# Optimization experiments

Measured on AMD Instinct MI355X. Metric: run time of the kernel, lower is better.

Reference implementation:

```python
import jax, jax.numpy as jnp
import numpy as np

B, S, L = 2, 2048, 2048
H, KVH, D = 16, 4, 128
HID = H * D
EPS = 1e-6
SCALE = 1.0 / np.sqrt(D)


def rmsnorm(x, w, eps=EPS):
    # normalize over last dim (head_size), fp32 math
    xf = x.astype(jnp.float32)
    var = jnp.mean(xf * xf, axis=-1, keepdims=True)
    return (xf * jax.lax.rsqrt(var + eps)).astype(x.dtype) * w


def setup_inputs() -> dict:
    key = jax.random.key(0)
    ks = jax.random.split(key, 5)
    s = 1.0 / np.sqrt(HID)
    return {
        "x": jax.random.normal(ks[0], (B, S, HID), jnp.float32),
        "c": jax.random.normal(ks[1], (B, L, HID), jnp.float32),
        "wq": jax.random.normal(ks[2], (HID, H * D), jnp.float32) * s,
        "wkv": jax.random.normal(ks[3], (HID, KVH * D * 2), jnp.float32) * s,
        "wo": jax.random.normal(ks[4], (H * D, HID), jnp.float32) * s,
        "norm_q_w": jnp.ones((D,), jnp.float32),
        "norm_k_w": jnp.ones((D,), jnp.float32),
    }


def reference(x, c, wq, wkv, wo, norm_q_w, norm_k_w):
    bs, seq_len, _ = x.shape
    c_len = c.shape[1]
    n_rep = H // KVH
    # Q projection + per-head RMSNorm
    xq = (x @ wq).reshape(bs, seq_len, H, D)
    xq = rmsnorm(xq, norm_q_w)
    # packed KV projection: view(..., kvh, hd, 2), unbind last dim
    ckv = (c @ wkv).reshape(bs, c_len, KVH, D, 2)
    ck, cv = ckv[..., 0], ckv[..., 1]
    ck = rmsnorm(ck, norm_k_w)
    # GQA repeat_kv (repeat_interleave over head dim)
    ck = jnp.repeat(ck, n_rep, axis=2)  # [b, L, H, D]
    cv = jnp.repeat(cv, n_rep, axis=2)
    # SDPA cross-attention, softmax in fp32
    scores = jnp.einsum("bqhd,bkhd->bhqk", xq, ck) * SCALE
    attn = jax.nn.softmax(scores.astype(jnp.float32), axis=-1).astype(xq.dtype)
    out = jnp.einsum("bhqk,bkhd->bqhd", attn, cv)
    out = out.reshape(bs, seq_len, H * D)
    return out @ wo
```

## Files before the change

### kernel.cpp

```cpp
#include <hip/hip_runtime.h>

#define B_ 2
#define S_ 2048
#define L_ 2048
#define H_ 16
#define KVH_ 4
#define D_ 128
#define HID_ 2048
#define EPS_ 1e-6f

typedef unsigned short u16;
typedef unsigned int u32;
typedef __bf16 bf16x8 __attribute__((ext_vector_type(8)));
typedef float f32x4 __attribute__((ext_vector_type(4)));
typedef unsigned u32x2v __attribute__((ext_vector_type(2)));
typedef unsigned u32x4v __attribute__((ext_vector_type(4)));

__device__ __forceinline__ float bf2f(u32 u) {
  union { u32 i; float f; } x; x.i = u << 16; return x.f;
}
__device__ __forceinline__ u16 f2bf(float f) {
  union { float f; u32 i; } x; x.f = f;
  return (u16)((x.i + 0x7fffu + ((x.i >> 16) & 1u)) >> 16);
}
__device__ __forceinline__ u32 pack_bf16(float a, float b) {
#if __has_builtin(__builtin_amdgcn_cvt_pk_bf16_f32)
  typedef __bf16 bf16x2 __attribute__((ext_vector_type(2)));
  union { bf16x2 v; u32 u; } c;
  c.v = __builtin_amdgcn_cvt_pk_bf16_f32(a, b);
  return c.u;
#else
  return (u32)f2bf(a) | ((u32)f2bf(b) << 16);
#endif
}
__device__ __forceinline__ void gl2lds16(const u16* g, u16* l) {
  __builtin_amdgcn_global_load_lds(
      (const __attribute__((address_space(1))) u32*)g,
      (__attribute__((address_space(3))) u32*)l, 16, 0, 0);
}

#if __has_builtin(__builtin_amdgcn_permlane32_swap) && __has_builtin(__builtin_amdgcn_permlane16_swap)
#define HAS_PLS 1
#else
#define HAS_PLS 0
#endif

__device__ __forceinline__ u32x4v ctoa(u32 xa, u32 xb, u32 ya, u32 yb,
                                       int quad, int l15) {
  u32x4v f;
#if HAS_PLS
  u32x2v t1 = __builtin_amdgcn_permlane32_swap(xa, ya, false, false);
  u32x2v t2 = __builtin_amdgcn_permlane16_swap(t1.x, t1.y, false, false);
  u32x2v t3 = __builtin_amdgcn_permlane32_swap(xb, yb, false, false);
  u32x2v t4 = __builtin_amdgcn_permlane16_swap(t3.x, t3.y, false, false);
  f.x = t2.x; f.y = t4.x; f.z = t2.y; f.w = t4.y;
#else
  int a0 = (((2 * quad) & 3) * 16 + l15) << 2;
  int a1 = (((2 * quad + 1) & 3) * 16 + l15) << 2;
  u32 xa0 = __builtin_amdgcn_ds_bpermute(a0, xa), ya0 = __builtin_amdgcn_ds_bpermute(a0, ya);
  u32 xb0 = __builtin_amdgcn_ds_bpermute(a0, xb), yb0 = __builtin_amdgcn_ds_bpermute(a0, yb);
  u32 xa1 = __builtin_amdgcn_ds_bpermute(a1, xa), ya1 = __builtin_amdgcn_ds_bpermute(a1, ya);
  u32 xb1 = __builtin_amdgcn_ds_bpermute(a1, xb), yb1 = __builtin_amdgcn_ds_bpermute(a1, yb);
  bool hi = quad >= 2;
  f.x = hi ? ya0 : xa0; f.y = hi ? yb0 : xb0;
  f.z = hi ? ya1 : xa1; f.w = hi ? yb1 : xb1;
#endif
  return f;
}

__global__ __launch_bounds__(256) void cvt_bf16(const float* __restrict__ in,
                                                u16* __restrict__ out, int n4) {
  int i = blockIdx.x * 256 + threadIdx.x;
  if (i >= n4) return;
  float4 v = ((const float4*)in)[i];
  uint2 o;
  o.x = pack_bf16(v.x, v.y);
  o.y = pack_bf16(v.z, v.w);
  ((uint2*)out)[i] = o;
}

__global__ __launch_bounds__(256) void transp_bf16(const float* __restrict__ A,
                                                   u16* __restrict__ At, int R, int C) {
  __shared__ float t[64][65];
  int c0 = blockIdx.x * 64, r0 = blockIdx.y * 64;
  int tx = threadIdx.x & 63, ty = threadIdx.x >> 6;
  for (int i = ty; i < 64; i += 4)
    t[i][tx] = A[(size_t)(r0 + i) * C + c0 + tx];
  __syncthreads();
  for (int i = ty; i < 64; i += 4)
    At[(size_t)(c0 + i) * R + r0 + tx] = f2bf(t[tx][i]);
}

__device__ __forceinline__ void store_out(u16* p, float v) { *p = f2bf(v); }
__device__ __forceinline__ void store_out(float* p, float v) { *p = v; }

template <typename OutT>
__global__ __launch_bounds__(256, 2) void gemm_bt(const u16* __restrict__ A,
                                                  const u16* __restrict__ Bt,
                                                  OutT* __restrict__ C,
                                                  int M, int N, int K) {
  __shared__ u16 sA[128 * 32];
  __shared__ u16 sB[128 * 32];
  const int tid = threadIdx.x;
  const int wave = tid >> 6, lane = tid & 63;
  const int quad = lane >> 4, l15 = lane & 15;
  const int m0 = blockIdx.x * 128, n0 = blockIdx.y * 128;
  const int wm = (wave >> 1) * 64, wn = (wave & 1) * 64;
  const u16* aP = A + (size_t)m0 * K;
  const u16* bP = Bt + (size_t)n0 * K;
  const int sr = lane >> 2;
  const int sc = (lane & 3) * 8;
  const int r0 = wave * 32, r1 = wave * 32 + 16;

  f32x4 acc[4][4];
  for (int i = 0; i < 4; i++)
    for (int j = 0; j < 4; j++)
      for (int r = 0; r < 4; r++) acc[i][j][r] = 0.0f;

  for (int k0 = 0; k0 < K; k0 += 32) {
    gl2lds16(aP + (size_t)(r0 + sr) * K + k0 + sc, &sA[r0 * 32]);
    gl2lds16(aP + (size_t)(r1 + sr) * K + k0 + sc, &sA[r1 * 32]);
    gl2lds16(bP + (size_t)(r0 + sr) * K + k0 + sc, &sB[r0 * 32]);
    gl2lds16(bP + (size_t)(r1 + sr) * K + k0 + sc, &sB[r1 * 32]);
    __syncthreads();
    bf16x8 afrag[4], bfrag[4];
    for (int i = 0; i < 4; i++)
      afrag[i] = *(const bf16x8*)&sA[(wm + i * 16 + l15) * 32 + quad * 8];
    for (int j = 0; j < 4; j++)
      bfrag[j] = *(const bf16x8*)&sB[(wn + j * 16 + l15) * 32 + quad * 8];
    for (int i = 0; i < 4; i++)
      for (int j = 0; j < 4; j++)
        acc[i][j] = __builtin_amdgcn_mfma_f32_16x16x32_bf16(afrag[i], bfrag[j], acc[i][j], 0, 0, 0);
    __syncthreads();
  }
  for (int i = 0; i < 4; i++)
    for (int j = 0; j < 4; j++) {
      int row = m0 + wm + i * 16 + quad * 4;
      int col = n0 + wn + j * 16 + l15;
      for (int r = 0; r < 4; r++)
        store_out(&C[(size_t)(row + r) * N + col], acc[i][j][r]);
    }
}

__global__ __launch_bounds__(256) void rmsnorm_q(u16* __restrict__ XQ,
                                                 const float* __restrict__ w) {
  int gw = blockIdx.x * 4 + (threadIdx.x >> 6);
  int lane = threadIdx.x & 63;
  u16* base = XQ + (size_t)gw * 128;
  float x0 = bf2f(base[lane]), x1 = bf2f(base[lane + 64]);
  float ss = x0 * x0 + x1 * x1;
  for (int off = 1; off < 64; off <<= 1) ss += __shfl_xor(ss, off);
  const float cexp = 0.12753102331322172f;
  float scale = rsqrtf(ss * (1.0f / 128.0f) + EPS_) * cexp;
  base[lane] = f2bf(x0 * scale * w[lane]);
  base[lane + 64] = f2bf(x1 * scale * w[lane + 64]);
}

__global__ __launch_bounds__(256) void knorm_deint(const u16* __restrict__ CKV,
                                                   const float* __restrict__ w,
                                                   u16* __restrict__ K,
                                                   u16* __restrict__ Vt) {
  __shared__ u16 vbuf[128][66];
  const int tid = threadIdx.x, wave = tid >> 6, lane = tid & 63;
  const int l0 = blockIdx.x * 64, kvh = blockIdx.y, b = blockIdx.z;
  for (int it = 0; it < 16; it++) {
    int ll = wave * 16 + it;
    int row = b * L_ + l0 + ll;
    const u16* src = CKV + (size_t)row * 1024 + kvh * 256;
    u32 p0 = *(const u32*)&src[lane * 2];
    u32 p1 = *(const u32*)&src[(lane + 64) * 2];
    float k0 = bf2f(p0 & 0xffff), v0 = bf2f(p0 >> 16);
    float k1 = bf2f(p1 & 0xffff), v1 = bf2f(p1 >> 16);
    float ss = k0 * k0 + k1 * k1;
    for (int off = 1; off < 64; off <<= 1) ss += __shfl_xor(ss, off);
    float sc = rsqrtf(ss * (1.0f / 128.0f) + EPS_);
    size_t kb = (((size_t)b * KVH_ + kvh) * L_ + l0 + ll) * D_;
    K[kb + lane] = f2bf(k0 * sc * w[lane]);
    K[kb + lane + 64] = f2bf(k1 * sc * w[lane + 64]);
    vbuf[lane][ll] = f2bf(v0);
    vbuf[lane + 64][ll] = f2bf(v1);
  }
  __syncthreads();
  for (int it = tid; it < 128 * 32; it += 256) {
    int d = it >> 5, cc = (it & 31) * 2;
    u32 pk = (u32)vbuf[d][cc] | ((u32)vbuf[d][cc + 1] << 16);
    *(u32*)&Vt[(((size_t)b * KVH_ + kvh) * D_ + d) * L_ + l0 + cc] = pk;
  }
}

__global__ __launch_bounds__(256, 4) void attn(const u16* __restrict__ Q,
                                               const u16* __restrict__ K,
                                               const u16* __restrict__ Vt,
                                               u16* __restrict__ AO) {
  __shared__ u16 sk[4][64 * 32];
  __shared__ u16 sv[2][128 * 32];
  const int tid = threadIdx.x, wave = tid >> 6, lane = tid & 63;
  const int quad = lane >> 4, l15 = lane & 15;
  const int qt = blockIdx.x, h = blockIdx.y, b = blockIdx.z;
  const int kvh = h >> 2;
  const int s0 = qt * 64, wr0 = wave * 16;

  const u16* qrow = Q + (size_t)(b * S_ + s0 + wr0 + l15) * HID_ + h * D_;
  bf16x8 qf[4];
  for (int kc = 0; kc < 4; kc++)
    qf[kc] = *(const bf16x8*)&qrow[kc * 32 + quad * 8];

  float psum = 0.0f;
  f32x4 o[8];
  for (int n = 0; n < 8; n++)
    for (int r = 0; r < 4; r++) o[n][r] = 0.0f;

  const u16* kbase = K + ((size_t)(b * KVH_ + kvh) * L_) * D_;
  const u16* vbase = Vt + ((size_t)(b * KVH_ + kvh) * D_) * L_;
  const int srow = lane >> 2, scol = (lane & 3) * 8;

  for (int l0 = 0; l0 < L_; l0 += 64) {
    const u16* kb = kbase + (size_t)l0 * D_ + wave * 32;
    for (int is = 0; is < 4; is++)
      gl2lds16(kb + (size_t)(is * 16 + srow) * D_ + scol, &sk[wave][is * 16 * 32]);
    const int c = wave >> 1;
    const u16* vb = vbase + l0 + c * 32;
    for (int j = 0; j < 4; j++) {
      int dr = (wave & 1) * 64 + j * 16;
      gl2lds16(vb + (size_t)(dr + srow) * L_ + scol, &sv[c][dr * 32]);
    }
    __syncthreads();

    f32x4 sacc[4];
    for (int j = 0; j < 4; j++)
      for (int r = 0; r < 4; r++) sacc[j][r] = 0.0f;
    for (int j = 0; j < 4; j++)
      for (int kc = 0; kc < 4; kc++) {
        bf16x8 kf = *(const bf16x8*)&sk[kc][(j * 16 + l15) * 32 + quad * 8];
        sacc[j] = __builtin_amdgcn_mfma_f32_16x16x32_bf16(kf, qf[kc], sacc[j], 0, 0, 0);
      }

    u32 pa[4], pb[4];
    for (int j = 0; j < 4; j++) {
      float p0 = exp2f(sacc[j][0]), p1 = exp2f(sacc[j][1]);
      float p2 = exp2f(sacc[j][2]), p3 = exp2f(sacc[j][3]);
      psum += (p0 + p1) + (p2 + p3);
      pa[j] = pack_bf16(p0, p1);
      pb[j] = pack_bf16(p2, p3);
    }

    for (int cc = 0; cc < 2; cc++) {
      union { u32x4v u; bf16x8 v; } pf;
      pf.u = ctoa(pa[2 * cc], pb[2 * cc], pa[2 * cc + 1], pb[2 * cc + 1], quad, l15);
      for (int n = 0; n < 8; n++) {
        bf16x8 vf = *(const bf16x8*)&sv[cc][(n * 16 + l15) * 32 + quad * 8];
        o[n] = __builtin_amdgcn_mfma_f32_16x16x32_bf16(pf.v, vf, o[n], 0, 0, 0);
      }
    }
    __syncthreads();
  }

  psum += __shfl_xor(psum, 16);
  psum += __shfl_xor(psum, 32);
  float linv = 1.0f / psum;
  float lr[4];
  for (int r = 0; r < 4; r++) lr[r] = __shfl(linv, quad * 4 + r);
  u16* ob = AO + (size_t)(b * S_ + s0 + wr0) * HID_ + h * D_;
  for (int n = 0; n < 8; n++)
    for (int r = 0; r < 4; r++)
      ob[(size_t)(quad * 4 + r) * HID_ + n * 16 + l15] = f2bf(o[n][r] * lr[r]);
}

extern "C" void kernel_launch(void* const* d_in, const int* in_sizes, int n_in,
                              void* d_out, int out_size, void* d_ws, size_t ws_size,
                              hipStream_t stream) {
  const float* x = (const float*)d_in[0];
  const float* c = (const float*)d_in[1];
  const float* wq = (const float*)d_in[2];
  const float* wkv = (const float*)d_in[3];
  const float* wo = (const float*)d_in[4];
  const float* nqw = (const float*)d_in[5];
  const float* nkw = (const float*)d_in[6];
  float* out = (float*)d_out;

  const int M = B_ * S_;
  char* p = (char*)d_ws;
  auto alloc = [&](size_t bytes) {
    char* r = p;
    p += (bytes + 255) & ~(size_t)255;
    return r;
  };
  u16* xbf = (u16*)alloc((size_t)M * HID_ * 2);
  u16* cbf = (u16*)alloc((size_t)M * HID_ * 2);
  u16* wqT = (u16*)alloc((size_t)HID_ * HID_ * 2);
  u16* wkvT = (u16*)alloc((size_t)1024 * HID_ * 2);
  u16* woT = (u16*)alloc((size_t)HID_ * HID_ * 2);
  u16* XQ = (u16*)alloc((size_t)M * HID_ * 2);
  u16* CKV = (u16*)alloc((size_t)M * 1024 * 2);
  u16* Kb = (u16*)alloc((size_t)B_ * KVH_ * L_ * D_ * 2);
  u16* Vt = (u16*)alloc((size_t)B_ * KVH_ * D_ * L_ * 2);
  u16* AO = (u16*)alloc((size_t)M * HID_ * 2);

  cvt_bf16<<<8192, 256, 0, stream>>>(x, xbf, M * HID_ / 4);
  cvt_bf16<<<8192, 256, 0, stream>>>(c, cbf, M * HID_ / 4);
  transp_bf16<<<dim3(32, 32), 256, 0, stream>>>(wq, wqT, HID_, HID_);
  transp_bf16<<<dim3(16, 32), 256, 0, stream>>>(wkv, wkvT, HID_, 1024);
  transp_bf16<<<dim3(32, 32), 256, 0, stream>>>(wo, woT, HID_, HID_);
  gemm_bt<u16><<<dim3(32, 16), 256, 0, stream>>>(xbf, wqT, XQ, M, HID_, HID_);
  gemm_bt<u16><<<dim3(32, 8), 256, 0, stream>>>(cbf, wkvT, CKV, M, 1024, HID_);
  rmsnorm_q<<<16384, 256, 0, stream>>>(XQ, nqw);
  knorm_deint<<<dim3(32, 4, 2), 256, 0, stream>>>(CKV, nkw, Kb, Vt);
  attn<<<dim3(32, 16, 2), 256, 0, stream>>>(XQ, Kb, Vt, AO);
  gemm_bt<float><<<dim3(32, 16), 256, 0, stream>>>(AO, woT, out, M, HID_, HID_);
}
```

Before: 419.7 us.

## Fuse Q RMSNorm into attention and double query/key tile per block

Result: faster. 401.2 us (-4.4%).

```diff
diff --git a/kernel.cpp b/kernel.cpp
--- a/kernel.cpp
+++ b/kernel.cpp
@@ -140,20 +140,6 @@
       for (int r = 0; r < 4; r++)
         store_out(&C[(size_t)(row + r) * N + col], acc[i][j][r]);
     }
-}
-
-__global__ __launch_bounds__(256) void rmsnorm_q(u16* __restrict__ XQ,
-                                                 const float* __restrict__ w) {
-  int gw = blockIdx.x * 4 + (threadIdx.x >> 6);
-  int lane = threadIdx.x & 63;
-  u16* base = XQ + (size_t)gw * 128;
-  float x0 = bf2f(base[lane]), x1 = bf2f(base[lane + 64]);
-  float ss = x0 * x0 + x1 * x1;
-  for (int off = 1; off < 64; off <<= 1) ss += __shfl_xor(ss, off);
-  const float cexp = 0.12753102331322172f;
-  float scale = rsqrtf(ss * (1.0f / 128.0f) + EPS_) * cexp;
-  base[lane] = f2bf(x0 * scale * w[lane]);
-  base[lane + 64] = f2bf(x1 * scale * w[lane + 64]);
 }
 
 __global__ __launch_bounds__(256) void knorm_deint(const u16* __restrict__ CKV,
@@ -188,82 +174,118 @@
   }
 }
 
-__global__ __launch_bounds__(256, 4) void attn(const u16* __restrict__ Q,
+__global__ __launch_bounds__(256, 2) void attn(const u16* __restrict__ XQ,
+                                               const float* __restrict__ nw,
                                                const u16* __restrict__ K,
                                                const u16* __restrict__ Vt,
                                                u16* __restrict__ AO) {
-  __shared__ u16 sk[4][64 * 32];
-  __shared__ u16 sv[2][128 * 32];
+  __shared__ u16 sk[4][128 * 32];
+  __shared__ u16 sv[4][128 * 32];
   const int tid = threadIdx.x, wave = tid >> 6, lane = tid & 63;
   const int quad = lane >> 4, l15 = lane & 15;
   const int qt = blockIdx.x, h = blockIdx.y, b = blockIdx.z;
   const int kvh = h >> 2;
-  const int s0 = qt * 64, wr0 = wave * 16;
-
-  const u16* qrow = Q + (size_t)(b * S_ + s0 + wr0 + l15) * HID_ + h * D_;
-  bf16x8 qf[4];
-  for (int kc = 0; kc < 4; kc++)
-    qf[kc] = *(const bf16x8*)&qrow[kc * 32 + quad * 8];
-
-  float psum = 0.0f;
-  f32x4 o[8];
-  for (int n = 0; n < 8; n++)
-    for (int r = 0; r < 4; r++) o[n][r] = 0.0f;
+  const int s0 = qt * 128, wr0 = wave * 32;
+
+  bf16x8 qf[2][4];
+  {
+    const float cexp = 0.12753102331322172f;
+    const u16* qrow = XQ + (size_t)(b * S_ + s0 + wr0 + l15) * HID_ + h * D_;
+    for (int i = 0; i < 2; i++) {
+      const u16* qr = qrow + (size_t)i * 16 * HID_;
+      float vals[4][8];
+      float ss = 0.0f;
+      for (int kc = 0; kc < 4; kc++) {
+        uint4 u = *(const uint4*)&qr[kc * 32 + quad * 8];
+        u32 uu[4] = {u.x, u.y, u.z, u.w};
+        for (int e = 0; e < 4; e++) {
+          float lo = bf2f(uu[e] & 0xffff), hi = bf2f(uu[e] >> 16);
+          vals[kc][2 * e] = lo;
+          vals[kc][2 * e + 1] = hi;
+          ss += lo * lo + hi * hi;
+        }
+      }
+      ss += __shfl_xor(ss, 16);
+      ss += __shfl_xor(ss, 32);
+      float scale = rsqrtf(ss * (1.0f / 128.0f) + EPS_) * cexp;
+      for (int kc = 0; kc < 4; kc++) {
+        float4 w0 = *(const float4*)&nw[kc * 32 + quad * 8];
+        float4 w1 = *(const float4*)&nw[kc * 32 + quad * 8 + 4];
+        union { u32x4v u; bf16x8 v; } q;
+        q.u.x = pack_bf16(vals[kc][0] * scale * w0.x, vals[kc][1] * scale * w0.y);
+        q.u.y = pack_bf16(vals[kc][2] * scale * w0.z, vals[kc][3] * scale * w0.w);
+        q.u.z = pack_bf16(vals[kc][4] * scale * w1.x, vals[kc][5] * scale * w1.y);
+        q.u.w = pack_bf16(vals[kc][6] * scale * w1.z, vals[kc][7] * scale * w1.w);
+        qf[i][kc] = q.v;
+      }
+    }
+  }
+
+  float psum[2] = {0.0f, 0.0f};
+  f32x4 o[2][8];
+  for (int i = 0; i < 2; i++)
+    for (int n = 0; n < 8; n++)
+      for (int r = 0; r < 4; r++) o[i][n][r] = 0.0f;
 
   const u16* kbase = K + ((size_t)(b * KVH_ + kvh) * L_) * D_;
   const u16* vbase = Vt + ((size_t)(b * KVH_ + kvh) * D_) * L_;
   const int srow = lane >> 2, scol = (lane & 3) * 8;
 
-  for (int l0 = 0; l0 < L_; l0 += 64) {
+  for (int l0 = 0; l0 < L_; l0 += 128) {
     const u16* kb = kbase + (size_t)l0 * D_ + wave * 32;
-    for (int is = 0; is < 4; is++)
+    for (int is = 0; is < 8; is++)
       gl2lds16(kb + (size_t)(is * 16 + srow) * D_ + scol, &sk[wave][is * 16 * 32]);
-    const int c = wave >> 1;
-    const u16* vb = vbase + l0 + c * 32;
-    for (int j = 0; j < 4; j++) {
-      int dr = (wave & 1) * 64 + j * 16;
-      gl2lds16(vb + (size_t)(dr + srow) * L_ + scol, &sv[c][dr * 32]);
+    const u16* vb = vbase + l0 + wave * 32;
+    for (int is = 0; is < 8; is++)
+      gl2lds16(vb + (size_t)(is * 16 + srow) * L_ + scol, &sv[wave][is * 16 * 32]);
+    __syncthreads();
+
+    for (int cc = 0; cc < 4; cc++) {
+      f32x4 sacc[2][2];
+      for (int jj = 0; jj < 2; jj++)
+        for (int i = 0; i < 2; i++)
+          for (int r = 0; r < 4; r++) sacc[jj][i][r] = 0.0f;
+      for (int jj = 0; jj < 2; jj++) {
+        int j = cc * 2 + jj;
+        for (int kc = 0; kc < 4; kc++) {
+          bf16x8 kf = *(const bf16x8*)&sk[kc][(j * 16 + l15) * 32 + quad * 8];
+          for (int i = 0; i < 2; i++)
+            sacc[jj][i] = __builtin_amdgcn_mfma_f32_16x16x32_bf16(kf, qf[i][kc], sacc[jj][i], 0, 0, 0);
+        }
+      }
+      union { u32x4v u; bf16x8 v; } pf[2];
+      for (int i = 0; i < 2; i++) {
+        float p0[4], p1[4];
+        for (int r = 0; r < 4; r++) {
+          p0[r] = exp2f(sacc[0][i][r]);
+          p1[r] = exp2f(sacc[1][i][r]);
+          psum[i] += p0[r] + p1[r];
+        }
+        u32 xa = pack_bf16(p0[0], p0[1]), xb = pack_bf16(p0[2], p0[3]);
+        u32 ya = pack_bf16(p1[0], p1[1]), yb = pack_bf16(p1[2], p1[3]);
+        pf[i].u = ctoa(xa, xb, ya, yb, quad, l15);
+      }
+      for (int n = 0; n < 8; n++) {
+        bf16x8 vf = *(const bf16x8*)&sv[cc][(n * 16 + l15) * 32 + quad * 8];
+        for (int i = 0; i < 2; i++)
+          o[i][n] = __builtin_amdgcn_mfma_f32_16x16x32_bf16(pf[i].v, vf, o[i][n], 0, 0, 0);
+      }
     }
     __syncthreads();
-
-    f32x4 sacc[4];
-    for (int j = 0; j < 4; j++)
-      for (int r = 0; r < 4; r++) sacc[j][r] = 0.0f;
-    for (int j = 0; j < 4; j++)
-      for (int kc = 0; kc < 4; kc++) {
-        bf16x8 kf = *(const bf16x8*)&sk[kc][(j * 16 + l15) * 32 + quad * 8];
-        sacc[j] = __builtin_amdgcn_mfma_f32_16x16x32_bf16(kf, qf[kc], sacc[j], 0, 0, 0);
-      }
-
-    u32 pa[4], pb[4];
-    for (int j = 0; j < 4; j++) {
-      float p0 = exp2f(sacc[j][0]), p1 = exp2f(sacc[j][1]);
-      float p2 = exp2f(sacc[j][2]), p3 = exp2f(sacc[j][3]);
-      psum += (p0 + p1) + (p2 + p3);
-      pa[j] = pack_bf16(p0, p1);
-      pb[j] = pack_bf16(p2, p3);
-    }
-
-    for (int cc = 0; cc < 2; cc++) {
-      union { u32x4v u; bf16x8 v; } pf;
-      pf.u = ctoa(pa[2 * cc], pb[2 * cc], pa[2 * cc + 1], pb[2 * cc + 1], quad, l15);
-      for (int n = 0; n < 8; n++) {
-        bf16x8 vf = *(const bf16x8*)&sv[cc][(n * 16 + l15) * 32 + quad * 8];
-        o[n] = __builtin_amdgcn_mfma_f32_16x16x32_bf16(pf.v, vf, o[n], 0, 0, 0);
-      }
-    }
-    __syncthreads();
-  }
-
-  psum += __shfl_xor(psum, 16);
-  psum += __shfl_xor(psum, 32);
-  float linv = 1.0f / psum;
-  float lr[4];
-  for (int r = 0; r < 4; r++) lr[r] = __shfl(linv, quad * 4 + r);
-  u16* ob = AO + (size_t)(b * S_ + s0 + wr0) * HID_ + h * D_;
-  for (int n = 0; n < 8; n++)
-    for (int r = 0; r < 4; r++)
-      ob[(size_t)(quad * 4 + r) * HID_ + n * 16 + l15] = f2bf(o[n][r] * lr[r]);
+  }
+
+  for (int i = 0; i < 2; i++) {
+    float s = psum[i];
+    s += __shfl_xor(s, 16);
+    s += __shfl_xor(s, 32);
+    float linv = 1.0f / s;
+    float lr[4];
+    for (int r = 0; r < 4; r++) lr[r] = __shfl(linv, quad * 4 + r);
+    u16* ob = AO + (size_t)(b * S_ + s0 + wr0 + i * 16) * HID_ + h * D_;
+    for (int n = 0; n < 8; n++)
+      for (int r = 0; r < 4; r++)
+        ob[(size_t)(quad * 4 + r) * HID_ + n * 16 + l15] = f2bf(o[i][n][r] * lr[r]);
+  }
 }
 
 extern "C" void kernel_launch(void* const* d_in, const int* in_sizes, int n_in,
@@ -303,8 +325,7 @@
   transp_bf16<<<dim3(32, 32), 256, 0, stream>>>(wo, woT, HID_, HID_);
   gemm_bt<u16><<<dim3(32, 16), 256, 0, stream>>>(xbf, wqT, XQ, M, HID_, HID_);
   gemm_bt<u16><<<dim3(32, 8), 256, 0, stream>>>(cbf, wkvT, CKV, M, 1024, HID_);
-  rmsnorm_q<<<16384, 256, 0, stream>>>(XQ, nqw);
   knorm_deint<<<dim3(32, 4, 2), 256, 0, stream>>>(CKV, nkw, Kb, Vt);
-  attn<<<dim3(32, 16, 2), 256, 0, stream>>>(XQ, Kb, Vt, AO);
+  attn<<<dim3(16, 16, 2), 256, 0, stream>>>(XQ, nqw, Kb, Vt, AO);
   gemm_bt<float><<<dim3(32, 16), 256, 0, stream>>>(AO, woT, out, M, HID_, HID_);
 }
```
